# Kernel optimization log

Measured on AMD Instinct MI355X. Metric: run time of the kernel, lower is better.

## Reference

```python
import jax, jax.numpy as jnp
import numpy as np

N, E, D, H = 50000, 800000, 128, 8
DH = D // H  # per-head out dim
DFF = 512


def setup_inputs() -> dict:
    key = jax.random.key(0)
    ks = jax.random.split(key, 8)
    return {
        "x": jax.random.normal(ks[0], (N, D), jnp.float32),
        "W_fc": jax.random.normal(ks[1], (H, D, DH), jnp.float32) * 0.05,
        "a_l": jax.random.normal(ks[2], (H, DH), jnp.float32) * 0.1,
        "a_r": jax.random.normal(ks[3], (H, DH), jnp.float32) * 0.1,
        "ln_gamma": jnp.ones((D,), jnp.float32),
        "ln_beta": jnp.zeros((D,), jnp.float32),
        "W1": jax.random.normal(ks[4], (D, DFF), jnp.float32) * 0.05,
        "b1": jnp.zeros((DFF,), jnp.float32),
        "W2": jax.random.normal(ks[5], (DFF, D), jnp.float32) * 0.05,
        "b2": jnp.zeros((D,), jnp.float32),
        "edge_src": jax.random.randint(ks[6], (E,), 0, N, jnp.int32),
        "edge_dst": jax.random.randint(ks[7], (E,), 0, N, jnp.int32),
    }


def _gat(x, W_fc, a_l, a_r, edge_src, edge_dst):
    # per-head linear projection: [N, H, DH]
    z = jnp.einsum('nd,hdk->nhk', x, W_fc)
    # attn_fc(cat[z_src, z_dst]) decomposed into left/right halves -> node-level terms
    el = jnp.einsum('nhk,hk->nh', z, a_l)  # [N, H]
    er = jnp.einsum('nhk,hk->nh', z, a_r)  # [N, H]
    e = jax.nn.leaky_relu(el[edge_src] + er[edge_dst], 0.01)  # [E, H]
    # segment softmax over incoming edges of each dst node
    m = jax.ops.segment_max(e, edge_dst, num_segments=N)      # [N, H]
    m = jnp.where(jnp.isfinite(m), m, 0.0)                    # empty segments -> -inf guard
    ee = jnp.exp(e - m[edge_dst])
    s = jax.ops.segment_sum(ee, edge_dst, num_segments=N)     # [N, H]
    alpha = ee / jnp.maximum(s[edge_dst], 1e-9)               # [E, H]
    # weighted scatter-aggregation of source features
    msg = alpha[:, :, None] * z[edge_src]                     # [E, H, DH]
    h = jax.ops.segment_sum(msg, edge_dst, num_segments=N)    # [N, H, DH]
    return h.reshape(N, H * DH)  # head concat -> [N, D]


def reference(x, W_fc, a_l, a_r, ln_gamma, ln_beta, W1, b1, W2, b2, edge_src, edge_dst):
    h = jax.nn.elu(_gat(x, W_fc, a_l, a_r, edge_src, edge_dst))
    h = x + h  # residual
    # PositionwiseFeedForward: LayerNorm -> Linear -> ReLU -> Linear -> residual
    mu = jnp.mean(h, axis=-1, keepdims=True)
    var = jnp.var(h, axis=-1, keepdims=True)
    ln = (h - mu) * jax.lax.rsqrt(var + 1e-5) * ln_gamma + ln_beta
    inter = jax.nn.relu(ln @ W1 + b1)
    return (inter @ W2 + b2) + h
```

## Files before the change

kernel.cpp:

```cpp
#include <hip/hip_runtime.h>
#include <math.h>

#define N_NODES 50000
#define E_EDGES 800000
#define D_DIM   128
#define H_HEADS 8
#define DH_DIM  16
#define DFF     512

#define SCAN_BLOCKS 98
#define FFN_GRID 256
#define NTILES 3125
#define PROJ_BLOCKS 782
#define FILL_BLOCKS 782

typedef __bf16 bf16_t;
typedef bf16_t bf16x8 __attribute__((ext_vector_type(8)));
typedef float f32x4 __attribute__((ext_vector_type(4)));
typedef unsigned short u16x8 __attribute__((ext_vector_type(8)));

#define SWZ(r) (((r) & 7) << 4)

__device__ __forceinline__ float lrelu(float v) { return v > 0.f ? v : 0.01f * v; }
__device__ __forceinline__ float elu(float v) { return v > 0.f ? v : __expf(v) - 1.f; }
__device__ __forceinline__ unsigned short f2b(float f) {
    unsigned u = __float_as_uint(f);
    unsigned r = (u + 0x7FFFu + ((u >> 16) & 1u)) >> 16;
    return (unsigned short)r;
}

__global__ void k_count(const int* __restrict__ ed, int* __restrict__ counts,
                        int* __restrict__ rank) {
    int e = blockIdx.x * 256 + threadIdx.x;
    if (e < E_EDGES) rank[e] = atomicAdd(&counts[ed[e]], 1);
}

__global__ __launch_bounds__(512) void k_scan1(const int* __restrict__ counts,
                                               int* __restrict__ bsum) {
    int i = blockIdx.x * 512 + threadIdx.x;
    int v = (i < N_NODES) ? counts[i] : 0;
    #pragma unroll
    for (int o = 1; o < 64; o <<= 1) v += __shfl_xor(v, o);
    __shared__ int ws[8];
    if ((threadIdx.x & 63) == 0) ws[threadIdx.x >> 6] = v;
    __syncthreads();
    if (threadIdx.x == 0) {
        int s = 0;
        #pragma unroll
        for (int k = 0; k < 8; ++k) s += ws[k];
        bsum[blockIdx.x] = s;
    }
}

__global__ __launch_bounds__(128) void k_scan2(const int* __restrict__ bsum,
                                               int* __restrict__ boff) {
    __shared__ int tmp[128];
    int t = threadIdx.x;
    int v = (t < SCAN_BLOCKS) ? bsum[t] : 0;
    tmp[t] = v;
    __syncthreads();
    for (int o = 1; o < 128; o <<= 1) {
        int u = (t >= o) ? tmp[t - o] : 0;
        __syncthreads();
        tmp[t] += u;
        __syncthreads();
    }
    boff[t] = (t == 0) ? 0 : tmp[t - 1];
}

__global__ __launch_bounds__(512) void k_scan3(const int* __restrict__ counts,
                                               const int* __restrict__ boff,
                                               int* __restrict__ csr_off) {
    int t = threadIdx.x;
    int i = blockIdx.x * 512 + t;
    int v = (i < N_NODES) ? counts[i] : 0;
    int lane = t & 63, w = t >> 6;
    int xs = v;
    #pragma unroll
    for (int o = 1; o < 64; o <<= 1) {
        int u = __shfl_up(xs, o);
        if (lane >= o) xs += u;
    }
    __shared__ int ws[8];
    __shared__ int wo[8];
    if (lane == 63) ws[w] = xs;
    __syncthreads();
    if (t == 0) {
        int s = 0;
        #pragma unroll
        for (int k = 0; k < 8; ++k) { wo[k] = s; s += ws[k]; }
    }
    __syncthreads();
    int excl = xs - v + wo[w] + boff[blockIdx.x];
    if (i < N_NODES) csr_off[i] = excl;
    if (i == N_NODES) csr_off[N_NODES] = E_EDGES;
}

__global__ void k_prep(const float* __restrict__ W1, const float* __restrict__ W2,
                       const float* __restrict__ Wfc,
                       bf16_t* __restrict__ W1T, bf16_t* __restrict__ W2T,
                       bf16_t* __restrict__ WpT, int* __restrict__ counts) {
    int id = blockIdx.x * 256 + threadIdx.x;
    if (id < N_NODES) counts[id] = 0;
    if (id < 512 * 128) {
        int c = id >> 7, k = id & 127;
        W1T[id] = (bf16_t)W1[(size_t)k * 512 + c];
        int c2 = id >> 9, k2 = id & 511;
        W2T[id] = (bf16_t)W2[(size_t)k2 * 128 + c2];
        if (id < 128 * 128) {
            int cp = id >> 7, kp = id & 127;
            WpT[id] = (bf16_t)Wfc[(cp >> 4) * 2048 + kp * 16 + (cp & 15)];
        }
    }
}

__global__ __launch_bounds__(512) void k_fillproj(const float* __restrict__ x,
                                                  const bf16_t* __restrict__ WpT,
                                                  const float* __restrict__ a_l,
                                                  const float* __restrict__ a_r,
                                                  unsigned short* __restrict__ zb,
                                                  float* __restrict__ el,
                                                  float* __restrict__ er,
                                                  const int* __restrict__ es,
                                                  const int* __restrict__ ed,
                                                  const int* __restrict__ rank,
                                                  const int* __restrict__ csr_off,
                                                  int* __restrict__ csr_src) {
    __shared__ char xbA[16384];
    int t = threadIdx.x;

    if (blockIdx.x >= PROJ_BLOCKS) {
        int e0 = (blockIdx.x - PROJ_BLOCKS) * 1024 + t;
        #pragma unroll
        for (int k = 0; k < 2; ++k) {
            int e = e0 + k * 512;
            if (e < E_EDGES) {
                int d = ed[e];
                csr_src[csr_off[d] + rank[e]] = es[e];
            }
        }
        return;
    }

    int r0 = blockIdx.x * 64;
    {
        int r = t >> 3, c0 = (t & 7) * 16;
        int gr = r0 + r;
        u16x8 pk0, pk1;
        if (gr < N_NODES) {
            #pragma unroll
            for (int q = 0; q < 2; ++q) {
                float4 a4 = *(const float4*)&x[(size_t)gr * 128 + c0 + q * 8];
                float4 b4 = *(const float4*)&x[(size_t)gr * 128 + c0 + q * 8 + 4];
                u16x8 pk;
                pk[0] = f2b(a4.x); pk[1] = f2b(a4.y); pk[2] = f2b(a4.z); pk[3] = f2b(a4.w);
                pk[4] = f2b(b4.x); pk[5] = f2b(b4.y); pk[6] = f2b(b4.z); pk[7] = f2b(b4.w);
                if (q == 0) pk0 = pk; else pk1 = pk;
            }
        } else {
            #pragma unroll
            for (int i = 0; i < 8; ++i) { pk0[i] = 0; pk1[i] = 0; }
        }
        int base = r * 256 + c0 * 2;
        *(u16x8*)(xbA + (base ^ SWZ(r))) = pk0;
        *(u16x8*)(xbA + ((base + 16) ^ SWZ(r))) = pk1;
    }
    __syncthreads();

    int wv = t >> 6, l = t & 63;
    int lr = l & 15, lg = l >> 4;

    f32x4 acc[4] = {};
    #pragma unroll
    for (int ks = 0; ks < 4; ++ks) {
        bf16x8 b = *(const bf16x8*)(WpT + (wv * 16 + lr) * 128 + ks * 32 + lg * 8);
        #pragma unroll
        for (int mi = 0; mi < 4; ++mi) {
            int row = mi * 16 + lr;
            int off = (row * 256 + ks * 64 + lg * 16) ^ SWZ(row);
            bf16x8 a = *(const bf16x8*)(xbA + off);
            acc[mi] = __builtin_amdgcn_mfma_f32_16x16x32_bf16(a, b, acc[mi], 0, 0, 0);
        }
    }

    float alv = a_l[wv * 16 + lr];
    float arv = a_r[wv * 16 + lr];
    float outL = 0.f, outR = 0.f;
    #pragma unroll
    for (int mi = 0; mi < 4; ++mi) {
        #pragma unroll
        for (int rg = 0; rg < 4; ++rg) {
            int row = mi * 16 + lg * 4 + rg;
            int grr = r0 + row;
            float v = acc[mi][rg];
            if (grr < N_NODES) zb[(size_t)grr * 128 + wv * 16 + lr] = f2b(v);
            float pl = v * alv, pr = v * arv;
            pl += __shfl_xor(pl, 1); pr += __shfl_xor(pr, 1);
            pl += __shfl_xor(pl, 2); pr += __shfl_xor(pr, 2);
            pl += __shfl_xor(pl, 4); pr += __shfl_xor(pr, 4);
            pl += __shfl_xor(pl, 8); pr += __shfl_xor(pr, 8);
            if (lr == mi * 4 + rg) { outL = pl; outR = pr; }
        }
    }
    int myrow = r0 + (lr >> 2) * 16 + lg * 4 + (lr & 3);
    if (myrow < N_NODES) {
        el[myrow * 8 + wv] = outL;
        er[myrow * 8 + wv] = outR;
    }
}

__global__ __launch_bounds__(256) void k_node(const int* __restrict__ csr_off,
                                              const int* __restrict__ csr_src,
                                              const float* __restrict__ el,
                                              const float* __restrict__ er,
                                              const unsigned short* __restrict__ zb,
                                              const float* __restrict__ x,
                                              const float* __restrict__ gamma,
                                              const float* __restrict__ beta,
                                              unsigned short* __restrict__ lnb,
                                              float* __restrict__ out) {
    int n = blockIdx.x * 8 + (threadIdx.x >> 5);
    int lane = threadIdx.x & 63;
    int q = lane & 31;
    int base = lane & 32;
    int h = q >> 2, s = q & 3;
    int row = csr_off[n];
    int deg = csr_off[n + 1] - row;
    float4 xv = *(const float4*)&x[(size_t)n * 128 + q * 4];
    float erv = er[n * 8 + h];
    int nch = (deg + 3) >> 2;

    float ps = 0.f;
    float ac0 = 0.f, ac1 = 0.f, ac2 = 0.f, ac3 = 0.f;
    const unsigned short* zbl = zb + q * 4;
    #pragma unroll
    for (int c = 0; c < 8; ++c) {
        if (c * 4 < deg) {
            int k = c * 4 + s;
            int kk = min(k, deg - 1);
            int src = csr_src[row + kk];
            float e = lrelu(el[src * 8 + h] + erv);
            float p = (k < deg) ? __expf(e) : 0.f;
            ps += p;
            float a[4];
            int se[4];
            #pragma unroll
            for (int tt = 0; tt < 4; ++tt) {
                a[tt] = __shfl(p, base + h * 4 + tt);
                se[tt] = __shfl(src, base + tt);
            }
            uint2 u[4];
            #pragma unroll
            for (int tt = 0; tt < 4; ++tt)
                u[tt] = *(const uint2*)(zbl + (size_t)se[tt] * 128);
            #pragma unroll
            for (int tt = 0; tt < 4; ++tt) {
                ac0 += a[tt] * __uint_as_float(u[tt].x << 16);
                ac1 += a[tt] * __uint_as_float(u[tt].x & 0xFFFF0000u);
                ac2 += a[tt] * __uint_as_float(u[tt].y << 16);
                ac3 += a[tt] * __uint_as_float(u[tt].y & 0xFFFF0000u);
            }
        }
    }
    for (int c = 8; c < nch; ++c) {
        int k = c * 4 + s;
        int kk = min(k, deg - 1);
        int src = csr_src[row + kk];
        float e = lrelu(el[src * 8 + h] + erv);
        float p = (k < deg) ? __expf(e) : 0.f;
        ps += p;
        float a[4];
        int se[4];
        #pragma unroll
        for (int tt = 0; tt < 4; ++tt) {
            a[tt] = __shfl(p, base + h * 4 + tt);
            se[tt] = __shfl(src, base + tt);
        }
        uint2 u[4];
        #pragma unroll
        for (int tt = 0; tt < 4; ++tt)
            u[tt] = *(const uint2*)(zbl + (size_t)se[tt] * 128);
        #pragma unroll
        for (int tt = 0; tt < 4; ++tt) {
            ac0 += a[tt] * __uint_as_float(u[tt].x << 16);
            ac1 += a[tt] * __uint_as_float(u[tt].x & 0xFFFF0000u);
            ac2 += a[tt] * __uint_as_float(u[tt].y << 16);
            ac3 += a[tt] * __uint_as_float(u[tt].y & 0xFFFF0000u);
        }
    }
    ps += __shfl_xor(ps, 1);
    ps += __shfl_xor(ps, 2);
    float inv = 1.f / fmaxf(ps, 1e-9f);
    float4 hv;
    hv.x = xv.x + elu(ac0 * inv);
    hv.y = xv.y + elu(ac1 * inv);
    hv.z = xv.z + elu(ac2 * inv);
    hv.w = xv.w + elu(ac3 * inv);
    *(float4*)&out[(size_t)n * 128 + q * 4] = hv;

    float rsm = hv.x + hv.y + hv.z + hv.w;
    float rsq = hv.x * hv.x + hv.y * hv.y + hv.z * hv.z + hv.w * hv.w;
    #pragma unroll
    for (int o = 1; o <= 16; o <<= 1) {
        rsm += __shfl_xor(rsm, o);
        rsq += __shfl_xor(rsq, o);
    }
    float mu = rsm * (1.f / 128.f);
    float rs = rsqrtf(rsq * (1.f / 128.f) - mu * mu + 1e-5f);
    float4 g4 = *(const float4*)&gamma[q * 4];
    float4 be4 = *(const float4*)&beta[q * 4];
    ushort4 pk;
    pk.x = f2b((hv.x - mu) * rs * g4.x + be4.x);
    pk.y = f2b((hv.y - mu) * rs * g4.y + be4.y);
    pk.z = f2b((hv.z - mu) * rs * g4.z + be4.z);
    pk.w = f2b((hv.w - mu) * rs * g4.w + be4.w);
    *(ushort4*)&lnb[(size_t)n * 128 + q * 4] = pk;
}

__global__ __launch_bounds__(256, 1) void k_ffn(const bf16_t* __restrict__ W1T,
                                                const float* __restrict__ b1,
                                                const bf16_t* __restrict__ W2T,
                                                const float* __restrict__ b2,
                                                const unsigned short* __restrict__ lnb,
                                                float* __restrict__ out) {
    __shared__ char inA[16384];
    int t = threadIdx.x;
    int w = t >> 6, l = t & 63;
    int lr = l & 15, lg = l >> 4;

    bf16x8 w1f[4][8];
    #pragma unroll
    for (int ks = 0; ks < 4; ++ks)
        #pragma unroll
        for (int tf = 0; tf < 8; ++tf)
            w1f[ks][tf] = *(const bf16x8*)(W1T + (size_t)(w * 128 + tf * 16 + lr) * 128 + ks * 32 + lg * 8);
    bf16x8 w2f[16][2];
    #pragma unroll
    for (int ks2 = 0; ks2 < 16; ++ks2)
        #pragma unroll
        for (int tc = 0; tc < 2; ++tc)
            w2f[ks2][tc] = *(const bf16x8*)(W2T + (size_t)(w * 32 + tc * 16 + lr) * 512 + ks2 * 32 + lg * 8);
    float4 b1v[8];
    #pragma unroll
    for (int tf = 0; tf < 8; ++tf)
        b1v[tf] = *(const float4*)&b1[w * 128 + tf * 16 + lg * 4];
    float4 b2v[2];
    #pragma unroll
    for (int tc = 0; tc < 2; ++tc)
        b2v[tc] = *(const float4*)&b2[w * 32 + tc * 16 + lg * 4];

    int tile = blockIdx.x;
    bf16x8 cur[4];
    #pragma unroll
    for (int ks = 0; ks < 4; ++ks)
        cur[ks] = *(const bf16x8*)(lnb + (size_t)(tile * 16 + lr) * 128 + ks * 32 + lg * 8);

    while (tile < NTILES) {
        float4 h4[2];
        #pragma unroll
        for (int tc = 0; tc < 2; ++tc)
            h4[tc] = *(const float4*)(out + (size_t)(tile * 16 + lr) * 128 + w * 32 + tc * 16 + lg * 4);

        f32x4 p[8] = {};
        #pragma unroll
        for (int ks = 0; ks < 4; ++ks)
            #pragma unroll
            for (int tf = 0; tf < 8; ++tf)
                p[tf] = __builtin_amdgcn_mfma_f32_16x16x32_bf16(w1f[ks][tf], cur[ks], p[tf], 0, 0, 0);

        int tn = tile + FFN_GRID;
        if (tn < NTILES) {
            #pragma unroll
            for (int ks = 0; ks < 4; ++ks)
                cur[ks] = *(const bf16x8*)(lnb + (size_t)(tn * 16 + lr) * 128 + ks * 32 + lg * 8);
        }

        #pragma unroll
        for (int tf = 0; tf < 8; ++tf) {
            float4 bb = b1v[tf];
            ushort4 pk;
            float v0 = p[tf][0] + bb.x; pk.x = f2b(v0 > 0.f ? v0 : 0.f);
            float v1 = p[tf][1] + bb.y; pk.y = f2b(v1 > 0.f ? v1 : 0.f);
            float v2 = p[tf][2] + bb.z; pk.z = f2b(v2 > 0.f ? v2 : 0.f);
            float v3 = p[tf][3] + bb.w; pk.w = f2b(v3 > 0.f ? v3 : 0.f);
            *(ushort4*)(inA + ((lr * 1024 + w * 256 + tf * 32 + lg * 8) ^ SWZ(lr))) = pk;
        }
        __syncthreads();

        f32x4 Q[2] = {};
        #pragma unroll
        for (int ks2 = 0; ks2 < 16; ++ks2) {
            bf16x8 bfr = *(const bf16x8*)(inA + ((lr * 1024 + ks2 * 64 + lg * 16) ^ SWZ(lr)));
            #pragma unroll
            for (int tc = 0; tc < 2; ++tc)
                Q[tc] = __builtin_amdgcn_mfma_f32_16x16x32_bf16(w2f[ks2][tc], bfr, Q[tc], 0, 0, 0);
        }

        #pragma unroll
        for (int tc = 0; tc < 2; ++tc) {
            float4 o4;
            o4.x = Q[tc][0] + b2v[tc].x + h4[tc].x;
            o4.y = Q[tc][1] + b2v[tc].y + h4[tc].y;
            o4.z = Q[tc][2] + b2v[tc].z + h4[tc].z;
            o4.w = Q[tc][3] + b2v[tc].w + h4[tc].w;
            *(float4*)(out + (size_t)(tile * 16 + lr) * 128 + w * 32 + tc * 16 + lg * 4) = o4;
        }
        __syncthreads();
        tile = tn;
    }
}

extern "C" void kernel_launch(void* const* d_in, const int* in_sizes, int n_in,
                              void* d_out, int out_size, void* d_ws, size_t ws_size,
                              hipStream_t stream) {
    const float* x     = (const float*)d_in[0];
    const float* Wfc   = (const float*)d_in[1];
    const float* a_l   = (const float*)d_in[2];
    const float* a_r   = (const float*)d_in[3];
    const float* gamma = (const float*)d_in[4];
    const float* beta  = (const float*)d_in[5];
    const float* W1    = (const float*)d_in[6];
    const float* b1    = (const float*)d_in[7];
    const float* W2    = (const float*)d_in[8];
    const float* b2    = (const float*)d_in[9];
    const int*   es    = (const int*)d_in[10];
    const int*   ed    = (const int*)d_in[11];
    float* out = (float*)d_out;

    bf16_t* W1T = (bf16_t*)d_ws;
    bf16_t* W2T = W1T + 512 * 128;
    bf16_t* WpT = W2T + 128 * 512;
    unsigned short* zb = (unsigned short*)(WpT + 128 * 128);
    float* el = (float*)(zb + (size_t)N_NODES * 128);
    float* er = el + N_NODES * 8;
    int* counts  = (int*)(er + N_NODES * 8);
    int* csr_off = counts + N_NODES;
    int* csr_src = csr_off + N_NODES + 1;
    int* rank    = csr_src + E_EDGES;
    int* bsum    = rank + E_EDGES;
    int* boff    = bsum + 128;
    unsigned short* lnbuf = (unsigned short*)(boff + 128);

    k_prep<<<dim3(256), dim3(256), 0, stream>>>(W1, W2, Wfc, W1T, W2T, WpT, counts);
    k_count<<<dim3((E_EDGES + 255) / 256), dim3(256), 0, stream>>>(ed, counts, rank);
    k_scan1<<<dim3(SCAN_BLOCKS), dim3(512), 0, stream>>>(counts, bsum);
    k_scan2<<<dim3(1), dim3(128), 0, stream>>>(bsum, boff);
    k_scan3<<<dim3(SCAN_BLOCKS), dim3(512), 0, stream>>>(counts, boff, csr_off);
    k_fillproj<<<dim3(PROJ_BLOCKS + FILL_BLOCKS), dim3(512), 0, stream>>>(
        x, WpT, a_l, a_r, zb, el, er, es, ed, rank, csr_off, csr_src);
    k_node<<<dim3(N_NODES / 8), dim3(256), 0, stream>>>(csr_off, csr_src, el, er, zb, x,
                                                        gamma, beta, lnbuf, out);
    k_ffn<<<dim3(FFN_GRID), dim3(256), 0, stream>>>(W1T, b1, W2T, b2, lnbuf, out);
}
```

Measured before the change: 153.1 us.

## Split node aggregation per head, transpose el/er, move LayerNorm into FFN

The attention-logit arrays el/er are stored head-major, and the aggregation kernel now assigns one head per block, with each half-wave handling a node for that head across five nodes per block. This is meant to give better cache locality for per-head gathers. LayerNorm moves from the node kernel into the FFN kernel, which reads h in fp32 and normalizes on the fly, removing the bf16 LN buffer write and read. In exchange, each edge's csr_src and el entries are now read 8 times (once per head), each gather is only 4 bytes, and the FFN loses its next-tile prefetch.

```diff
diff --git a/kernel.cpp b/kernel.cpp
--- a/kernel.cpp
+++ b/kernel.cpp
@@ -13,6 +13,8 @@
 #define NTILES 3125
 #define PROJ_BLOCKS 782
 #define FILL_BLOCKS 782
+#define NODE_ITERS 5
+#define KNODE_GRID 10000
 
 typedef __bf16 bf16_t;
 typedef bf16_t bf16x8 __attribute__((ext_vector_type(8)));
@@ -119,8 +121,8 @@
                                                   const float* __restrict__ a_l,
                                                   const float* __restrict__ a_r,
                                                   unsigned short* __restrict__ zb,
-                                                  float* __restrict__ el,
-                                                  float* __restrict__ er,
+                                                  float* __restrict__ elT,
+                                                  float* __restrict__ erT,
                                                   const int* __restrict__ es,
                                                   const int* __restrict__ ed,
                                                   const int* __restrict__ rank,
@@ -204,124 +206,80 @@
     }
     int myrow = r0 + (lr >> 2) * 16 + lg * 4 + (lr & 3);
     if (myrow < N_NODES) {
-        el[myrow * 8 + wv] = outL;
-        er[myrow * 8 + wv] = outR;
+        elT[(size_t)wv * N_NODES + myrow] = outL;
+        erT[(size_t)wv * N_NODES + myrow] = outR;
     }
 }
 
 __global__ __launch_bounds__(256) void k_node(const int* __restrict__ csr_off,
                                               const int* __restrict__ csr_src,
-                                              const float* __restrict__ el,
-                                              const float* __restrict__ er,
+                                              const float* __restrict__ elT,
+                                              const float* __restrict__ erT,
                                               const unsigned short* __restrict__ zb,
                                               const float* __restrict__ x,
-                                              const float* __restrict__ gamma,
-                                              const float* __restrict__ beta,
-                                              unsigned short* __restrict__ lnb,
                                               float* __restrict__ out) {
-    int n = blockIdx.x * 8 + (threadIdx.x >> 5);
-    int lane = threadIdx.x & 63;
-    int q = lane & 31;
-    int base = lane & 32;
-    int h = q >> 2, s = q & 3;
-    int row = csr_off[n];
-    int deg = csr_off[n + 1] - row;
-    float4 xv = *(const float4*)&x[(size_t)n * 128 + q * 4];
-    float erv = er[n * 8 + h];
-    int nch = (deg + 3) >> 2;
-
-    float ps = 0.f;
-    float ac0 = 0.f, ac1 = 0.f, ac2 = 0.f, ac3 = 0.f;
-    const unsigned short* zbl = zb + q * 4;
-    #pragma unroll
-    for (int c = 0; c < 8; ++c) {
-        if (c * 4 < deg) {
+    int h = blockIdx.x & 7;
+    int grp = blockIdx.x >> 3;
+    int t = threadIdx.x;
+    int hw = t >> 5;
+    int q = t & 31;
+    int s = q >> 3, dp = q & 7;
+    const float* elh = elT + (size_t)h * N_NODES;
+    const float* erh = erT + (size_t)h * N_NODES;
+    const unsigned short* zbh = zb + h * 16 + dp * 2;
+
+    for (int it = 0; it < NODE_ITERS; ++it) {
+        int n = (grp * NODE_ITERS + it) * 8 + hw;
+        int row = csr_off[n];
+        int deg = csr_off[n + 1] - row;
+        float erv = erh[n];
+        float ps = 0.f, a0 = 0.f, a1 = 0.f;
+        #pragma unroll
+        for (int c = 0; c < 8; ++c) {
+            if (c * 4 < deg) {
+                int k = c * 4 + s;
+                int kk = min(k, deg - 1);
+                int src = csr_src[row + kk];
+                float e = lrelu(elh[src] + erv);
+                float p = (k < deg) ? __expf(e) : 0.f;
+                ps += p;
+                unsigned u = *(const unsigned*)(zbh + (size_t)src * 128);
+                a0 += p * __uint_as_float(u << 16);
+                a1 += p * __uint_as_float(u & 0xFFFF0000u);
+            }
+        }
+        int nch = (deg + 3) >> 2;
+        for (int c = 8; c < nch; ++c) {
             int k = c * 4 + s;
             int kk = min(k, deg - 1);
             int src = csr_src[row + kk];
-            float e = lrelu(el[src * 8 + h] + erv);
+            float e = lrelu(elh[src] + erv);
             float p = (k < deg) ? __expf(e) : 0.f;
             ps += p;
-            float a[4];
-            int se[4];
-            #pragma unroll
-            for (int tt = 0; tt < 4; ++tt) {
-                a[tt] = __shfl(p, base + h * 4 + tt);
-                se[tt] = __shfl(src, base + tt);
-            }
-            uint2 u[4];
-            #pragma unroll
-            for (int tt = 0; tt < 4; ++tt)
-                u[tt] = *(const uint2*)(zbl + (size_t)se[tt] * 128);
-            #pragma unroll
-            for (int tt = 0; tt < 4; ++tt) {
-                ac0 += a[tt] * __uint_as_float(u[tt].x << 16);
-                ac1 += a[tt] * __uint_as_float(u[tt].x & 0xFFFF0000u);
-                ac2 += a[tt] * __uint_as_float(u[tt].y << 16);
-                ac3 += a[tt] * __uint_as_float(u[tt].y & 0xFFFF0000u);
-            }
-        }
-    }
-    for (int c = 8; c < nch; ++c) {
-        int k = c * 4 + s;
-        int kk = min(k, deg - 1);
-        int src = csr_src[row + kk];
-        float e = lrelu(el[src * 8 + h] + erv);
-        float p = (k < deg) ? __expf(e) : 0.f;
-        ps += p;
-        float a[4];
-        int se[4];
-        #pragma unroll
-        for (int tt = 0; tt < 4; ++tt) {
-            a[tt] = __shfl(p, base + h * 4 + tt);
-            se[tt] = __shfl(src, base + tt);
-        }
-        uint2 u[4];
-        #pragma unroll
-        for (int tt = 0; tt < 4; ++tt)
-            u[tt] = *(const uint2*)(zbl + (size_t)se[tt] * 128);
-        #pragma unroll
-        for (int tt = 0; tt < 4; ++tt) {
-            ac0 += a[tt] * __uint_as_float(u[tt].x << 16);
-            ac1 += a[tt] * __uint_as_float(u[tt].x & 0xFFFF0000u);
-            ac2 += a[tt] * __uint_as_float(u[tt].y << 16);
-            ac3 += a[tt] * __uint_as_float(u[tt].y & 0xFFFF0000u);
-        }
-    }
-    ps += __shfl_xor(ps, 1);
-    ps += __shfl_xor(ps, 2);
-    float inv = 1.f / fmaxf(ps, 1e-9f);
-    float4 hv;
-    hv.x = xv.x + elu(ac0 * inv);
-    hv.y = xv.y + elu(ac1 * inv);
-    hv.z = xv.z + elu(ac2 * inv);
-    hv.w = xv.w + elu(ac3 * inv);
-    *(float4*)&out[(size_t)n * 128 + q * 4] = hv;
-
-    float rsm = hv.x + hv.y + hv.z + hv.w;
-    float rsq = hv.x * hv.x + hv.y * hv.y + hv.z * hv.z + hv.w * hv.w;
-    #pragma unroll
-    for (int o = 1; o <= 16; o <<= 1) {
-        rsm += __shfl_xor(rsm, o);
-        rsq += __shfl_xor(rsq, o);
-    }
-    float mu = rsm * (1.f / 128.f);
-    float rs = rsqrtf(rsq * (1.f / 128.f) - mu * mu + 1e-5f);
-    float4 g4 = *(const float4*)&gamma[q * 4];
-    float4 be4 = *(const float4*)&beta[q * 4];
-    ushort4 pk;
-    pk.x = f2b((hv.x - mu) * rs * g4.x + be4.x);
-    pk.y = f2b((hv.y - mu) * rs * g4.y + be4.y);
-    pk.z = f2b((hv.z - mu) * rs * g4.z + be4.z);
-    pk.w = f2b((hv.w - mu) * rs * g4.w + be4.w);
-    *(ushort4*)&lnb[(size_t)n * 128 + q * 4] = pk;
+            unsigned u = *(const unsigned*)(zbh + (size_t)src * 128);
+            a0 += p * __uint_as_float(u << 16);
+            a1 += p * __uint_as_float(u & 0xFFFF0000u);
+        }
+        ps += __shfl_xor(ps, 8);  ps += __shfl_xor(ps, 16);
+        a0 += __shfl_xor(a0, 8);  a0 += __shfl_xor(a0, 16);
+        a1 += __shfl_xor(a1, 8);  a1 += __shfl_xor(a1, 16);
+        if (s == 0) {
+            float inv = 1.f / fmaxf(ps, 1e-9f);
+            float2 xv = *(const float2*)&x[(size_t)n * 128 + h * 16 + dp * 2];
+            float2 hv;
+            hv.x = xv.x + elu(a0 * inv);
+            hv.y = xv.y + elu(a1 * inv);
+            *(float2*)&out[(size_t)n * 128 + h * 16 + dp * 2] = hv;
+        }
+    }
 }
 
 __global__ __launch_bounds__(256, 1) void k_ffn(const bf16_t* __restrict__ W1T,
                                                 const float* __restrict__ b1,
                                                 const bf16_t* __restrict__ W2T,
                                                 const float* __restrict__ b2,
-                                                const unsigned short* __restrict__ lnb,
+                                                const float* __restrict__ gamma,
+                                                const float* __restrict__ beta,
                                                 float* __restrict__ out) {
     __shared__ char inA[16384];
     int t = threadIdx.x;
@@ -350,16 +308,43 @@
         b2v[tc] = *(const float4*)&b2[w * 32 + tc * 16 + lg * 4];
 
     int tile = blockIdx.x;
-    bf16x8 cur[4];
-    #pragma unroll
-    for (int ks = 0; ks < 4; ++ks)
-        cur[ks] = *(const bf16x8*)(lnb + (size_t)(tile * 16 + lr) * 128 + ks * 32 + lg * 8);
-
     while (tile < NTILES) {
+        const float* hbase = out + (size_t)(tile * 16 + lr) * 128;
         float4 h4[2];
         #pragma unroll
         for (int tc = 0; tc < 2; ++tc)
-            h4[tc] = *(const float4*)(out + (size_t)(tile * 16 + lr) * 128 + w * 32 + tc * 16 + lg * 4);
+            h4[tc] = *(const float4*)(hbase + w * 32 + tc * 16 + lg * 4);
+
+        float hvv[4][8];
+        float sm = 0.f, sq = 0.f;
+        #pragma unroll
+        for (int ks = 0; ks < 4; ++ks) {
+            float4 A = *(const float4*)(hbase + ks * 32 + lg * 8);
+            float4 B = *(const float4*)(hbase + ks * 32 + lg * 8 + 4);
+            hvv[ks][0] = A.x; hvv[ks][1] = A.y; hvv[ks][2] = A.z; hvv[ks][3] = A.w;
+            hvv[ks][4] = B.x; hvv[ks][5] = B.y; hvv[ks][6] = B.z; hvv[ks][7] = B.w;
+            #pragma unroll
+            for (int j = 0; j < 8; ++j) { sm += hvv[ks][j]; sq += hvv[ks][j] * hvv[ks][j]; }
+        }
+        sm += __shfl_xor(sm, 16); sq += __shfl_xor(sq, 16);
+        sm += __shfl_xor(sm, 32); sq += __shfl_xor(sq, 32);
+        float mu = sm * (1.f / 128.f);
+        float rs = rsqrtf(sq * (1.f / 128.f) - mu * mu + 1e-5f);
+        bf16x8 cur[4];
+        #pragma unroll
+        for (int ks = 0; ks < 4; ++ks) {
+            float4 g0 = *(const float4*)&gamma[ks * 32 + lg * 8];
+            float4 g1 = *(const float4*)&gamma[ks * 32 + lg * 8 + 4];
+            float4 be0 = *(const float4*)&beta[ks * 32 + lg * 8];
+            float4 be1 = *(const float4*)&beta[ks * 32 + lg * 8 + 4];
+            float ga[8] = {g0.x, g0.y, g0.z, g0.w, g1.x, g1.y, g1.z, g1.w};
+            float ba[8] = {be0.x, be0.y, be0.z, be0.w, be1.x, be1.y, be1.z, be1.w};
+            u16x8 pk;
+            #pragma unroll
+            for (int j = 0; j < 8; ++j)
+                pk[j] = f2b((hvv[ks][j] - mu) * rs * ga[j] + ba[j]);
+            cur[ks] = __builtin_bit_cast(bf16x8, pk);
+        }
 
         f32x4 p[8] = {};
         #pragma unroll
@@ -367,13 +352,6 @@
             #pragma unroll
             for (int tf = 0; tf < 8; ++tf)
                 p[tf] = __builtin_amdgcn_mfma_f32_16x16x32_bf16(w1f[ks][tf], cur[ks], p[tf], 0, 0, 0);
-
-        int tn = tile + FFN_GRID;
-        if (tn < NTILES) {
-            #pragma unroll
-            for (int ks = 0; ks < 4; ++ks)
-                cur[ks] = *(const bf16x8*)(lnb + (size_t)(tn * 16 + lr) * 128 + ks * 32 + lg * 8);
-        }
 
         #pragma unroll
         for (int tf = 0; tf < 8; ++tf) {
@@ -406,7 +384,7 @@
             *(float4*)(out + (size_t)(tile * 16 + lr) * 128 + w * 32 + tc * 16 + lg * 4) = o4;
         }
         __syncthreads();
-        tile = tn;
+        tile += FFN_GRID;
     }
 }
 
@@ -431,15 +409,14 @@
     bf16_t* W2T = W1T + 512 * 128;
     bf16_t* WpT = W2T + 128 * 512;
     unsigned short* zb = (unsigned short*)(WpT + 128 * 128);
-    float* el = (float*)(zb + (size_t)N_NODES * 128);
-    float* er = el + N_NODES * 8;
-    int* counts  = (int*)(er + N_NODES * 8);
+    float* elT = (float*)(zb + (size_t)N_NODES * 128);
+    float* erT = elT + (size_t)8 * N_NODES;
+    int* counts  = (int*)(erT + (size_t)8 * N_NODES);
     int* csr_off = counts + N_NODES;
     int* csr_src = csr_off + N_NODES + 1;
     int* rank    = csr_src + E_EDGES;
     int* bsum    = rank + E_EDGES;
     int* boff    = bsum + 128;
-    unsigned short* lnbuf = (unsigned short*)(boff + 128);
 
     k_prep<<<dim3(256), dim3(256), 0, stream>>>(W1, W2, Wfc, W1T, W2T, WpT, counts);
     k_count<<<dim3((E_EDGES + 255) / 256), dim3(256), 0, stream>>>(ed, counts, rank);
@@ -447,8 +424,7 @@
     k_scan2<<<dim3(1), dim3(128), 0, stream>>>(bsum, boff);
     k_scan3<<<dim3(SCAN_BLOCKS), dim3(512), 0, stream>>>(counts, boff, csr_off);
     k_fillproj<<<dim3(PROJ_BLOCKS + FILL_BLOCKS), dim3(512), 0, stream>>>(
-        x, WpT, a_l, a_r, zb, el, er, es, ed, rank, csr_off, csr_src);
-    k_node<<<dim3(N_NODES / 8), dim3(256), 0, stream>>>(csr_off, csr_src, el, er, zb, x,
-                                                        gamma, beta, lnbuf, out);
-    k_ffn<<<dim3(FFN_GRID), dim3(256), 0, stream>>>(W1T, b1, W2T, b2, lnbuf, out);
-}
+        x, WpT, a_l, a_r, zb, elT, erT, es, ed, rank, csr_off, csr_src);
+    k_node<<<dim3(KNODE_GRID), dim3(256), 0, stream>>>(csr_off, csr_src, elT, erT, zb, x, out);
+    k_ffn<<<dim3(FFN_GRID), dim3(256), 0, stream>>>(W1T, b1, W2T, b2, gamma, beta, out);
+}
```

Result: slower. 251.8 us (+64.4%).
